# Optimization experiments

Hardware: AMD Instinct MI355X
Metric: run time of the kernel (lower is better)

The kernel has to match this reference:

```python
import jax, jax.numpy as jnp
import numpy as np

NUM_HEADS = 64          # also the positional-embedding size (quirk of the module)
DIM_IN, DIM_K, DIM_V = 512, 512, 64
BATCH, SEQ = 4, 1024


def setup_inputs() -> dict:
    key = jax.random.key(0)
    ks = jax.random.split(key, 7)
    s = 0.05  # weight init scale
    return {
        "x":  jax.random.normal(ks[0], (BATCH, SEQ, DIM_IN), jnp.float32),
        "Wq": jax.random.normal(ks[1], (DIM_IN, DIM_K), jnp.float32) * s,
        "bq": jax.random.normal(ks[2], (DIM_K,), jnp.float32) * s,
        "Wk": jax.random.normal(ks[3], (DIM_IN, DIM_K), jnp.float32) * s,
        "bk": jax.random.normal(ks[4], (DIM_K,), jnp.float32) * s,
        "Wv": jax.random.normal(ks[5], (DIM_IN, DIM_V), jnp.float32) * s,
        "bv": jax.random.normal(ks[6], (DIM_V,), jnp.float32) * s,
    }


def _position_embedding(n, position_size):
    # matches Position_Enbedding: cos block then sin block along feature dim
    half = position_size // 2
    pos_j = 1.0 / jnp.power(10000.0, 2.0 * jnp.arange(half, dtype=jnp.float32) / position_size)
    pos_ij = jnp.arange(n, dtype=jnp.float32)[:, None] * pos_j[None, :]   # [n, half]
    return jnp.concatenate([jnp.cos(pos_ij), jnp.sin(pos_ij)], axis=1)    # [n, position_size]


def reference(x, Wq, bq, Wk, bk, Wv, bv):
    B, n, _ = x.shape
    nh = NUM_HEADS
    dk = DIM_K // nh   # 8
    dv = DIM_V // nh   # 1
    # fused linear + ReLU, then split heads: [B, nh, n, d]
    q = jax.nn.relu(x @ Wq + bq).reshape(B, n, nh, dk).transpose(0, 2, 1, 3)
    k = jax.nn.relu(x @ Wk + bk).reshape(B, n, nh, dk).transpose(0, 2, 1, 3)
    v = jax.nn.relu(x @ Wv + bv).reshape(B, n, nh, dv).transpose(0, 2, 1, 3)
    scale = 1.0 / np.sqrt(dk).astype(np.float32)
    dist = jax.nn.softmax(jnp.einsum('bhqd,bhkd->bhqk', q, k) * scale, axis=-1)
    att = jnp.einsum('bhqk,bhkd->bhqd', dist, v)            # [B, nh, n, dv]
    att = att.transpose(0, 2, 1, 3).reshape(B, n, DIM_V)    # [B, n, dim_v]
    pe = _position_embedding(n, nh)                          # [n, nh] == [n, dim_v]
    return att + pe[None, :, :]
```

## Files before the change

kernel.cpp:

```cpp
#include <hip/hip_runtime.h>
#include <math.h>

#define BATCH 4
#define SEQ   1024
#define DIN   512
#define DKQ   512
#define DV    64
#define NH    64

typedef __attribute__((ext_vector_type(8))) short short8v;
typedef __attribute__((ext_vector_type(4))) float float4v;
typedef __attribute__((ext_vector_type(4))) unsigned int uint4v;

__device__ __forceinline__ void split_bf16(float f, unsigned short& hi, unsigned short& lo) {
    unsigned int u = __float_as_uint(f);
    hi = (unsigned short)(u >> 16);
    float l = f - __uint_as_float(u & 0xFFFF0000u);
    lo = (unsigned short)(__float_as_uint(l) >> 16);
}
__device__ __forceinline__ unsigned short f32_to_bf16_rne(float f) {
    unsigned int u = __float_as_uint(f);
    u += 0x7FFFu + ((u >> 16) & 1u);
    return (unsigned short)(u >> 16);
}
__device__ __forceinline__ float bf16_bits_to_f32(unsigned short s) {
    return __uint_as_float((unsigned int)s << 16);
}

__device__ __forceinline__ int ldsoff(int r, int sl) {
    return r * 64 + ((sl ^ (r & 7)) << 3);
}

__global__ __launch_bounds__(256)
void pack_x(const float* __restrict__ x,
            unsigned short* __restrict__ Xhi, unsigned short* __restrict__ Xlo)
{
    const int i = (blockIdx.x * 256 + threadIdx.x) * 8;
    float4 a0 = *(const float4*)&x[i];
    float4 a1 = *(const float4*)&x[i + 4];
    float av[8] = {a0.x, a0.y, a0.z, a0.w, a1.x, a1.y, a1.z, a1.w};
    short8v h, l;
    #pragma unroll
    for (int j = 0; j < 8; ++j) {
        unsigned short hh, ll; split_bf16(av[j], hh, ll);
        h[j] = (short)hh; l[j] = (short)ll;
    }
    *(short8v*)&Xhi[i] = h;
    *(short8v*)&Xlo[i] = l;
}

__global__ __launch_bounds__(256)
void transpose_w(const float* __restrict__ Wq, const float* __restrict__ Wk,
                 const float* __restrict__ Wv,
                 unsigned short* __restrict__ WhiQ, unsigned short* __restrict__ WloQ,
                 unsigned short* __restrict__ WhiK, unsigned short* __restrict__ WloK,
                 unsigned short* __restrict__ WhiV, unsigned short* __restrict__ WloV)
{
    const int z = blockIdx.z;
    const int N = (z == 2) ? DV : DKQ;
    if (z == 2 && blockIdx.x >= 2) return;
    const float* __restrict__ W = (z == 0) ? Wq : (z == 1) ? Wk : Wv;
    unsigned short* __restrict__ Whi = (z == 0) ? WhiQ : (z == 1) ? WhiK : WhiV;
    unsigned short* __restrict__ Wlo = (z == 0) ? WloQ : (z == 1) ? WloK : WloV;

    __shared__ float tile[32][33];
    const int n0 = blockIdx.x * 32, k0 = blockIdx.y * 32;
    const int tx = threadIdx.x, ty = threadIdx.y;
    #pragma unroll
    for (int i = 0; i < 32; i += 8)
        tile[ty + i][tx] = W[(size_t)(k0 + ty + i) * N + n0 + tx];
    __syncthreads();
    #pragma unroll
    for (int i = 0; i < 32; i += 8) {
        unsigned short h, l; split_bf16(tile[tx][ty + i], h, l);
        Whi[(size_t)(n0 + ty + i) * DIN + k0 + tx] = h;
        Wlo[(size_t)(n0 + ty + i) * DIN + k0 + tx] = l;
    }
}

__global__ __launch_bounds__(512)
void proj_kernel(const unsigned short* __restrict__ Xhi,
                 const unsigned short* __restrict__ Xlo,
                 const unsigned short* __restrict__ WhiQ, const unsigned short* __restrict__ WloQ,
                 const float* __restrict__ bq,
                 const unsigned short* __restrict__ WhiK, const unsigned short* __restrict__ WloK,
                 const float* __restrict__ bk,
                 const unsigned short* __restrict__ WhiV, const unsigned short* __restrict__ WloV,
                 const float* __restrict__ bv,
                 unsigned short* __restrict__ Qpk, unsigned short* __restrict__ Kpk,
                 unsigned int* __restrict__ Vhi, unsigned int* __restrict__ Vlo)
{
    const int z = blockIdx.z;
    if (z == 2 && blockIdx.x != 0) return;
    const unsigned short* __restrict__ Whi = (z == 0) ? WhiQ : (z == 1) ? WhiK : WhiV;
    const unsigned short* __restrict__ Wlo = (z == 0) ? WloQ : (z == 1) ? WloK : WloV;
    const float* __restrict__ bias = (z == 0) ? bq : (z == 1) ? bk : bv;

    __shared__ unsigned short As[128 * 64];
    __shared__ unsigned short Bs[128 * 64];

    const int t  = threadIdx.x;
    const int bm = blockIdx.y * 128;
    const int bn = blockIdx.x * 128;

    const int srow = t >> 2;
    const int sg   = t & 3;
    const bool bok = (z != 2) || (srow < 64);

    const int lane = t & 63, wave = t >> 6;
    const int wr = wave >> 2, wc = wave & 3;
    const int cl = lane & 15, g2 = lane >> 4;
    const int NF = (z == 2) ? 1 : 2;

    float4v acc[4][2];
    #pragma unroll
    for (int i = 0; i < 4; ++i)
        #pragma unroll
        for (int j = 0; j < 2; ++j)
            acc[i][j] = (float4v){0.f, 0.f, 0.f, 0.f};

    for (int ks = 0; ks < 16; ++ks) {
        const int k0 = ks * 32;
        const size_t ao = (size_t)(bm + srow) * DIN + k0 + sg * 8;
        short8v ahi = *(const short8v*)(Xhi + ao);
        short8v alo = *(const short8v*)(Xlo + ao);
        short8v bhi, blo;
        if (bok) {
            const size_t bo = (size_t)(bn + srow) * DIN + k0 + sg * 8;
            bhi = *(const short8v*)(Whi + bo);
            blo = *(const short8v*)(Wlo + bo);
        }
        __syncthreads();
        *(short8v*)&As[ldsoff(srow, sg * 2)]     = ahi;
        *(short8v*)&As[ldsoff(srow, sg * 2 + 1)] = alo;
        if (bok) {
            *(short8v*)&Bs[ldsoff(srow, sg * 2)]     = bhi;
            *(short8v*)&Bs[ldsoff(srow, sg * 2 + 1)] = blo;
        }
        __syncthreads();

        short8v af_h[4], af_l[4], bf_h[2], bf_l[2];
        #pragma unroll
        for (int mt = 0; mt < 4; ++mt) {
            const int r = wr * 64 + mt * 16 + cl;
            af_h[mt] = *(const short8v*)&As[ldsoff(r, g2 * 2)];
            af_l[mt] = *(const short8v*)&As[ldsoff(r, g2 * 2 + 1)];
        }
        #pragma unroll
        for (int nf = 0; nf < 2; ++nf) {
            if (nf < NF) {
                const int n = wc * (NF * 16) + nf * 16 + cl;
                bf_h[nf] = *(const short8v*)&Bs[ldsoff(n, g2 * 2)];
                bf_l[nf] = *(const short8v*)&Bs[ldsoff(n, g2 * 2 + 1)];
            }
        }
        #pragma unroll
        for (int mt = 0; mt < 4; ++mt)
            #pragma unroll
            for (int nf = 0; nf < 2; ++nf) {
                if (nf >= NF) continue;
                acc[mt][nf] = __builtin_amdgcn_mfma_f32_16x16x32_bf16(af_h[mt], bf_h[nf], acc[mt][nf], 0, 0, 0);
                acc[mt][nf] = __builtin_amdgcn_mfma_f32_16x16x32_bf16(af_l[mt], bf_h[nf], acc[mt][nf], 0, 0, 0);
                acc[mt][nf] = __builtin_amdgcn_mfma_f32_16x16x32_bf16(af_h[mt], bf_l[nf], acc[mt][nf], 0, 0, 0);
            }
    }

    const float cc = 0.35355339059327373f * 1.4426950408889634f;
    if (z == 2) {
        const int n = wc * 16 + cl;
        #pragma unroll
        for (int mt = 0; mt < 4; ++mt) {
            float vv[4]; unsigned short hh[4], ll[4];
            #pragma unroll
            for (int r = 0; r < 4; ++r) {
                vv[r] = fmaxf(acc[mt][0][r] + bias[n], 0.0f);
                hh[r] = f32_to_bf16_rne(vv[r]);
                ll[r] = f32_to_bf16_rne(vv[r] - bf16_bits_to_f32(hh[r]));
            }
            const int row0 = bm + wr * 64 + mt * 16 + g2 * 4;
            const int bb = row0 >> 10, s0 = row0 & 1023;
            size_t base = (size_t)((bb << 6) + n) * (SEQ / 2) + (s0 >> 1);
            Vhi[base]     = (unsigned int)hh[0] | ((unsigned int)hh[1] << 16);
            Vhi[base + 1] = (unsigned int)hh[2] | ((unsigned int)hh[3] << 16);
            Vlo[base]     = (unsigned int)ll[0] | ((unsigned int)ll[1] << 16);
            Vlo[base + 1] = (unsigned int)ll[2] | ((unsigned int)ll[3] << 16);
        }
    } else {
        #pragma unroll
        for (int mt = 0; mt < 4; ++mt) {
            #pragma unroll
            for (int nf = 0; nf < 2; ++nf) {
                #pragma unroll
                for (int r = 0; r < 4; ++r) {
                    const int row = bm + wr * 64 + mt * 16 + g2 * 4 + r;
                    const int bb = row >> 10, s = row & 1023;
                    const int n = bn + wc * 32 + nf * 16 + cl;
                    float val = fmaxf(acc[mt][nf][r] + bias[n], 0.0f);
                    if (z == 0) val *= cc;
                    const int hh2 = n >> 3, d = n & 7;
                    unsigned short* dst = (z == 0) ? Qpk : Kpk;
                    size_t base = ((size_t)((bb << 6) + hh2) * SEQ + s) * 16 + d;
                    unsigned short hi = f32_to_bf16_rne(val);
                    dst[base]     = hi;
                    dst[base + 8] = f32_to_bf16_rne(val - bf16_bits_to_f32(hi));
                }
            }
        }
    }
}

__global__ __launch_bounds__(256, 6)
void attn_kernel(const unsigned short* __restrict__ Qpk,
                 const unsigned short* __restrict__ Kpk,
                 const unsigned int* __restrict__ Vhi,
                 const unsigned int* __restrict__ Vlo,
                 float2* __restrict__ part)
{
    const int bh = blockIdx.x;
    const int yb = blockIdx.y;
    const int qchunk = yb >> 2;
    const int kq = yb & 3;
    const int t = threadIdx.x;
    const int wave = t >> 6, lane = t & 63;
    const int g = lane >> 4, cl = lane & 15;

    const unsigned short* __restrict__ qb = Qpk + (size_t)bh * SEQ * 16;
    const unsigned short* __restrict__ kb = Kpk + (size_t)bh * SEQ * 16;
    const unsigned int* __restrict__ vhb = Vhi + (size_t)bh * (SEQ / 2);
    const unsigned int* __restrict__ vlb = Vlo + (size_t)bh * (SEQ / 2);

    const int q0 = qchunk * 256 + wave * 64;

    short8v bq[4];
    #pragma unroll
    for (int qt = 0; qt < 4; ++qt) {
        if (g == 3) { short8v zz = {0,0,0,0,0,0,0,0}; bq[qt] = zz; }
        else bq[qt] = *(const short8v*)(qb + (size_t)(q0 + qt * 16 + cl) * 16 + ((g == 1) ? 8 : 0));
    }

    const int koff = (g >> 1) * 8;
    const unsigned int ONES = 0x3F803F80u;
    const float4v c0 = {0.f, 0.f, 0.f, 0.f};

    float4v acc[4];
    #pragma unroll
    for (int qt = 0; qt < 4; ++qt) acc[qt] = c0;

    const int nt0 = kq * 16;
    short8v kf = *(const short8v*)(kb + (size_t)(nt0 * 16 + cl) * 16 + koff);
    unsigned int vh0 = vhb[nt0 * 8 + g * 2], vh1 = vhb[nt0 * 8 + g * 2 + 1];
    unsigned int vl0 = vlb[nt0 * 8 + g * 2], vl1 = vlb[nt0 * 8 + g * 2 + 1];

    for (int nt = nt0; nt < nt0 + 16; ++nt) {
        const short8v kfc = kf;
        const unsigned int ch0 = vh0, ch1 = vh1, cll0 = vl0, cll1 = vl1;
        if (nt < nt0 + 15) {
            kf = *(const short8v*)(kb + (size_t)((nt + 1) * 16 + cl) * 16 + koff);
            vh0 = vhb[(nt + 1) * 8 + g * 2]; vh1 = vhb[(nt + 1) * 8 + g * 2 + 1];
            vl0 = vlb[(nt + 1) * 8 + g * 2]; vl1 = vlb[(nt + 1) * 8 + g * 2 + 1];
        }
        const unsigned int a0 = (cl == 0) ? ch0 : (cl == 1) ? ONES : (cl == 2) ? cll0 : 0u;
        const unsigned int a1 = (cl == 0) ? ch1 : (cl == 1) ? ONES : (cl == 2) ? cll1 : 0u;
        uint4v au = {a0, a1, 0u, 0u};
        const short8v af = __builtin_bit_cast(short8v, au);

        #pragma unroll
        for (int qt = 0; qt < 4; ++qt) {
            float4v st = __builtin_amdgcn_mfma_f32_16x16x32_bf16(kfc, bq[qt], c0, 0, 0, 0);
            float p0 = __builtin_amdgcn_exp2f(st[0]);
            float p1 = __builtin_amdgcn_exp2f(st[1]);
            float p2 = __builtin_amdgcn_exp2f(st[2]);
            float p3 = __builtin_amdgcn_exp2f(st[3]);
            unsigned int pk0 = __builtin_amdgcn_perm(__float_as_uint(p1), __float_as_uint(p0), 0x07060302u);
            unsigned int pk1 = __builtin_amdgcn_perm(__float_as_uint(p3), __float_as_uint(p2), 0x07060302u);
            uint4v pu = {pk0, pk1, 0u, 0u};
            acc[qt] = __builtin_amdgcn_mfma_f32_16x16x32_bf16(af, __builtin_bit_cast(short8v, pu), acc[qt], 0, 0, 0);
        }
    }

    if (g == 0) {
        #pragma unroll
        for (int qt = 0; qt < 4; ++qt) {
            const int row = q0 + qt * 16 + cl;
            float2 pr;
            pr.x = acc[qt][0] + acc[qt][2];
            pr.y = acc[qt][1];
            part[(size_t)(kq * 256 + bh) * SEQ + row] = pr;
        }
    }
}

__global__ __launch_bounds__(256)
void merge_kernel(const float2* __restrict__ part, float* __restrict__ out)
{
    const int tid = blockIdx.x * 256 + threadIdx.x;
    const int h = tid & 63;
    const int q = (tid >> 6) & 1023;
    const int b = tid >> 16;
    const int bh = (b << 6) + h;
    float num = 0.f, den = 0.f;
    #pragma unroll
    for (int kq = 0; kq < 4; ++kq) {
        float2 p = part[(size_t)(kq * 256 + bh) * SEQ + q];
        num += p.x; den += p.y;
    }
    const float fr = __builtin_amdgcn_exp2f((float)(h & 31) * -0.4152410118609203f);
    const float pe = (h < 32) ? cosf((float)q * fr) : sinf((float)q * fr);
    out[tid] = num / den + pe;
}

extern "C" void kernel_launch(void* const* d_in, const int* in_sizes, int n_in,
                              void* d_out, int out_size, void* d_ws, size_t ws_size,
                              hipStream_t stream)
{
    const float* x  = (const float*)d_in[0];
    const float* Wq = (const float*)d_in[1];
    const float* bq = (const float*)d_in[2];
    const float* Wk = (const float*)d_in[3];
    const float* bk = (const float*)d_in[4];
    const float* Wv = (const float*)d_in[5];
    const float* bv = (const float*)d_in[6];
    float* out = (float*)d_out;

    unsigned short* Qpk = (unsigned short*)d_ws;
    unsigned short* Kpk = Qpk + (size_t)BATCH * NH * SEQ * 16;
    unsigned int* Vhi = (unsigned int*)(Kpk + (size_t)BATCH * NH * SEQ * 16);
    unsigned int* Vlo = Vhi + (size_t)BATCH * NH * (SEQ / 2);
    unsigned short* Xhi = (unsigned short*)(Vlo + (size_t)BATCH * NH * (SEQ / 2));
    unsigned short* Xlo = Xhi + (size_t)BATCH * SEQ * DIN;
    float2* part = (float2*)Xhi;
    unsigned short* WhiQ = Xlo + (size_t)BATCH * SEQ * DIN;
    unsigned short* WloQ = WhiQ + (size_t)DIN * DKQ;
    unsigned short* WhiK = WloQ + (size_t)DIN * DKQ;
    unsigned short* WloK = WhiK + (size_t)DIN * DKQ;
    unsigned short* WhiV = WloK + (size_t)DIN * DKQ;
    unsigned short* WloV = WhiV + (size_t)DIN * DV;

    pack_x<<<dim3((BATCH * SEQ * DIN) / (8 * 256)), 256, 0, stream>>>(x, Xhi, Xlo);
    transpose_w<<<dim3(16, 16, 3), dim3(32, 8), 0, stream>>>(
        Wq, Wk, Wv, WhiQ, WloQ, WhiK, WloK, WhiV, WloV);
    proj_kernel<<<dim3(4, 32, 3), 512, 0, stream>>>(
        Xhi, Xlo, WhiQ, WloQ, bq, WhiK, WloK, bk, WhiV, WloV, bv, Qpk, Kpk, Vhi, Vlo);
    attn_kernel<<<dim3(256, 16), 256, 0, stream>>>(Qpk, Kpk, Vhi, Vlo, part);
    merge_kernel<<<dim3((BATCH * SEQ * DV) / 256), 256, 0, stream>>>(part, out);
}
```

Before: 86.18 us.

## Drop LDS staging in projection GEMM and process two key tiles per attention step

After: 115.8 us. 34.4% more time.

```diff
diff --git a/kernel.cpp b/kernel.cpp
--- a/kernel.cpp
+++ b/kernel.cpp
@@ -27,14 +27,13 @@
     return __uint_as_float((unsigned int)s << 16);
 }
 
-__device__ __forceinline__ int ldsoff(int r, int sl) {
-    return r * 64 + ((sl ^ (r & 7)) << 3);
-}
-
 __global__ __launch_bounds__(256)
 void pack_x(const float* __restrict__ x,
-            unsigned short* __restrict__ Xhi, unsigned short* __restrict__ Xlo)
-{
+            unsigned short* __restrict__ Xhi, unsigned short* __restrict__ Xlo,
+            unsigned int* __restrict__ obuf)
+{
+    if (blockIdx.x == 0 && threadIdx.x < 8)
+        obuf[threadIdx.x] = (threadIdx.x < 4) ? 0x3F803F80u : 0u;
     const int i = (blockIdx.x * 256 + threadIdx.x) * 8;
     float4 a0 = *(const float4*)&x[i];
     float4 a1 = *(const float4*)&x[i + 4];
@@ -78,7 +77,7 @@
     }
 }
 
-__global__ __launch_bounds__(512)
+__global__ __launch_bounds__(256)
 void proj_kernel(const unsigned short* __restrict__ Xhi,
                  const unsigned short* __restrict__ Xlo,
                  const unsigned short* __restrict__ WhiQ, const unsigned short* __restrict__ WloQ,
@@ -88,118 +87,125 @@
                  const unsigned short* __restrict__ WhiV, const unsigned short* __restrict__ WloV,
                  const float* __restrict__ bv,
                  unsigned short* __restrict__ Qpk, unsigned short* __restrict__ Kpk,
-                 unsigned int* __restrict__ Vhi, unsigned int* __restrict__ Vlo)
+                 unsigned int* __restrict__ Vsh, unsigned int* __restrict__ Vsl)
 {
     const int z = blockIdx.z;
-    if (z == 2 && blockIdx.x != 0) return;
+    const int t = threadIdx.x;
+    const int wave = t >> 6, lane = t & 63;
+    const int cl = lane & 15, g2 = lane >> 4;
+
+    int bm, cb;
+    if (z == 2) {
+        if (blockIdx.x != 0 || blockIdx.y >= 16) return;
+        bm = blockIdx.y * 256 + wave * 64;
+        cb = 0;
+    } else {
+        bm = blockIdx.y * 64;
+        cb = blockIdx.x * 256 + wave * 64;
+    }
     const unsigned short* __restrict__ Whi = (z == 0) ? WhiQ : (z == 1) ? WhiK : WhiV;
     const unsigned short* __restrict__ Wlo = (z == 0) ? WloQ : (z == 1) ? WloK : WloV;
     const float* __restrict__ bias = (z == 0) ? bq : (z == 1) ? bk : bv;
 
-    __shared__ unsigned short As[128 * 64];
-    __shared__ unsigned short Bs[128 * 64];
-
-    const int t  = threadIdx.x;
-    const int bm = blockIdx.y * 128;
-    const int bn = blockIdx.x * 128;
-
-    const int srow = t >> 2;
-    const int sg   = t & 3;
-    const bool bok = (z != 2) || (srow < 64);
-
-    const int lane = t & 63, wave = t >> 6;
-    const int wr = wave >> 2, wc = wave & 3;
-    const int cl = lane & 15, g2 = lane >> 4;
-    const int NF = (z == 2) ? 1 : 2;
-
-    float4v acc[4][2];
+    unsigned int aoff[4], boff[4];
+    #pragma unroll
+    for (int mt = 0; mt < 4; ++mt) aoff[mt] = (unsigned)(bm + mt * 16 + cl) * DIN + g2 * 8;
+    #pragma unroll
+    for (int nf = 0; nf < 4; ++nf) boff[nf] = (unsigned)(cb + nf * 16 + cl) * DIN + g2 * 8;
+
+    float4v acc[4][4];
     #pragma unroll
     for (int i = 0; i < 4; ++i)
         #pragma unroll
-        for (int j = 0; j < 2; ++j)
+        for (int j = 0; j < 4; ++j)
             acc[i][j] = (float4v){0.f, 0.f, 0.f, 0.f};
 
+    short8v Ah[2][4], Al[2][4], Bh[2][4], Bl[4];
+    #pragma unroll
+    for (int mt = 0; mt < 4; ++mt) {
+        Ah[0][mt] = *(const short8v*)(Xhi + aoff[mt]);
+        Al[0][mt] = *(const short8v*)(Xlo + aoff[mt]);
+    }
+    #pragma unroll
+    for (int nf = 0; nf < 4; ++nf)
+        Bh[0][nf] = *(const short8v*)(Whi + boff[nf]);
+
+    #pragma unroll
     for (int ks = 0; ks < 16; ++ks) {
-        const int k0 = ks * 32;
-        const size_t ao = (size_t)(bm + srow) * DIN + k0 + sg * 8;
-        short8v ahi = *(const short8v*)(Xhi + ao);
-        short8v alo = *(const short8v*)(Xlo + ao);
-        short8v bhi, blo;
-        if (bok) {
-            const size_t bo = (size_t)(bn + srow) * DIN + k0 + sg * 8;
-            bhi = *(const short8v*)(Whi + bo);
-            blo = *(const short8v*)(Wlo + bo);
-        }
-        __syncthreads();
-        *(short8v*)&As[ldsoff(srow, sg * 2)]     = ahi;
-        *(short8v*)&As[ldsoff(srow, sg * 2 + 1)] = alo;
-        if (bok) {
-            *(short8v*)&Bs[ldsoff(srow, sg * 2)]     = bhi;
-            *(short8v*)&Bs[ldsoff(srow, sg * 2 + 1)] = blo;
-        }
-        __syncthreads();
-
-        short8v af_h[4], af_l[4], bf_h[2], bf_l[2];
-        #pragma unroll
-        for (int mt = 0; mt < 4; ++mt) {
-            const int r = wr * 64 + mt * 16 + cl;
-            af_h[mt] = *(const short8v*)&As[ldsoff(r, g2 * 2)];
-            af_l[mt] = *(const short8v*)&As[ldsoff(r, g2 * 2 + 1)];
-        }
-        #pragma unroll
-        for (int nf = 0; nf < 2; ++nf) {
-            if (nf < NF) {
-                const int n = wc * (NF * 16) + nf * 16 + cl;
-                bf_h[nf] = *(const short8v*)&Bs[ldsoff(n, g2 * 2)];
-                bf_l[nf] = *(const short8v*)&Bs[ldsoff(n, g2 * 2 + 1)];
+        const int cur = ks & 1, nxt = cur ^ 1;
+        const int ko = ks * 32;
+        #pragma unroll
+        for (int nf = 0; nf < 4; ++nf)
+            Bl[nf] = *(const short8v*)(Wlo + boff[nf] + ko);
+        if (ks < 15) {
+            const int kn = ko + 32;
+            #pragma unroll
+            for (int mt = 0; mt < 4; ++mt) {
+                Ah[nxt][mt] = *(const short8v*)(Xhi + aoff[mt] + kn);
+                Al[nxt][mt] = *(const short8v*)(Xlo + aoff[mt] + kn);
             }
+            #pragma unroll
+            for (int nf = 0; nf < 4; ++nf)
+                Bh[nxt][nf] = *(const short8v*)(Whi + boff[nf] + kn);
         }
         #pragma unroll
         for (int mt = 0; mt < 4; ++mt)
             #pragma unroll
-            for (int nf = 0; nf < 2; ++nf) {
-                if (nf >= NF) continue;
-                acc[mt][nf] = __builtin_amdgcn_mfma_f32_16x16x32_bf16(af_h[mt], bf_h[nf], acc[mt][nf], 0, 0, 0);
-                acc[mt][nf] = __builtin_amdgcn_mfma_f32_16x16x32_bf16(af_l[mt], bf_h[nf], acc[mt][nf], 0, 0, 0);
-                acc[mt][nf] = __builtin_amdgcn_mfma_f32_16x16x32_bf16(af_h[mt], bf_l[nf], acc[mt][nf], 0, 0, 0);
-            }
+            for (int nf = 0; nf < 4; ++nf)
+                acc[mt][nf] = __builtin_amdgcn_mfma_f32_16x16x32_bf16(Ah[cur][mt], Bh[cur][nf], acc[mt][nf], 0, 0, 0);
+        #pragma unroll
+        for (int mt = 0; mt < 4; ++mt)
+            #pragma unroll
+            for (int nf = 0; nf < 4; ++nf)
+                acc[mt][nf] = __builtin_amdgcn_mfma_f32_16x16x32_bf16(Al[cur][mt], Bh[cur][nf], acc[mt][nf], 0, 0, 0);
+        #pragma unroll
+        for (int mt = 0; mt < 4; ++mt)
+            #pragma unroll
+            for (int nf = 0; nf < 4; ++nf)
+                acc[mt][nf] = __builtin_amdgcn_mfma_f32_16x16x32_bf16(Ah[cur][mt], Bl[nf], acc[mt][nf], 0, 0, 0);
     }
 
     const float cc = 0.35355339059327373f * 1.4426950408889634f;
     if (z == 2) {
-        const int n = wc * 16 + cl;
         #pragma unroll
         for (int mt = 0; mt < 4; ++mt) {
-            float vv[4]; unsigned short hh[4], ll[4];
-            #pragma unroll
-            for (int r = 0; r < 4; ++r) {
-                vv[r] = fmaxf(acc[mt][0][r] + bias[n], 0.0f);
-                hh[r] = f32_to_bf16_rne(vv[r]);
-                ll[r] = f32_to_bf16_rne(vv[r] - bf16_bits_to_f32(hh[r]));
-            }
-            const int row0 = bm + wr * 64 + mt * 16 + g2 * 4;
+            const int row0 = bm + mt * 16 + g2 * 4;
             const int bb = row0 >> 10, s0 = row0 & 1023;
-            size_t base = (size_t)((bb << 6) + n) * (SEQ / 2) + (s0 >> 1);
-            Vhi[base]     = (unsigned int)hh[0] | ((unsigned int)hh[1] << 16);
-            Vhi[base + 1] = (unsigned int)hh[2] | ((unsigned int)hh[3] << 16);
-            Vlo[base]     = (unsigned int)ll[0] | ((unsigned int)ll[1] << 16);
-            Vlo[base + 1] = (unsigned int)ll[2] | ((unsigned int)ll[3] << 16);
-        }
-    } else {
-        #pragma unroll
-        for (int mt = 0; mt < 4; ++mt) {
-            #pragma unroll
-            for (int nf = 0; nf < 2; ++nf) {
+            const int idx0 = (s0 >> 5) * 16 + ((s0 >> 2) & 3) * 4 + ((s0 >> 4) & 1) * 2;
+            #pragma unroll
+            for (int nf = 0; nf < 4; ++nf) {
+                const int n = nf * 16 + cl;
+                const float bn = bias[n];
+                float vv[4]; unsigned short hh[4], ll[4];
                 #pragma unroll
                 for (int r = 0; r < 4; ++r) {
-                    const int row = bm + wr * 64 + mt * 16 + g2 * 4 + r;
+                    vv[r] = fmaxf(acc[mt][nf][r] + bn, 0.0f);
+                    hh[r] = f32_to_bf16_rne(vv[r]);
+                    ll[r] = f32_to_bf16_rne(vv[r] - bf16_bits_to_f32(hh[r]));
+                }
+                const size_t base = (size_t)((bb << 6) + n) * 512 + idx0;
+                Vsh[base]     = (unsigned int)hh[0] | ((unsigned int)hh[1] << 16);
+                Vsh[base + 1] = (unsigned int)hh[2] | ((unsigned int)hh[3] << 16);
+                Vsl[base]     = (unsigned int)ll[0] | ((unsigned int)ll[1] << 16);
+                Vsl[base + 1] = (unsigned int)ll[2] | ((unsigned int)ll[3] << 16);
+            }
+        }
+    } else {
+        unsigned short* __restrict__ dst = (z == 0) ? Qpk : Kpk;
+        #pragma unroll
+        for (int nf = 0; nf < 4; ++nf) {
+            const int n = cb + nf * 16 + cl;
+            const float bn = bias[n];
+            const int h = n >> 3, d = n & 7;
+            #pragma unroll
+            for (int mt = 0; mt < 4; ++mt) {
+                #pragma unroll
+                for (int r = 0; r < 4; ++r) {
+                    const int row = bm + mt * 16 + g2 * 4 + r;
                     const int bb = row >> 10, s = row & 1023;
-                    const int n = bn + wc * 32 + nf * 16 + cl;
-                    float val = fmaxf(acc[mt][nf][r] + bias[n], 0.0f);
+                    float val = fmaxf(acc[mt][nf][r] + bn, 0.0f);
                     if (z == 0) val *= cc;
-                    const int hh2 = n >> 3, d = n & 7;
-                    unsigned short* dst = (z == 0) ? Qpk : Kpk;
-                    size_t base = ((size_t)((bb << 6) + hh2) * SEQ + s) * 16 + d;
+                    const size_t base = ((size_t)((bb << 6) + h) * SEQ + s) * 16 + d;
                     unsigned short hi = f32_to_bf16_rne(val);
                     dst[base]     = hi;
                     dst[base + 8] = f32_to_bf16_rne(val - bf16_bits_to_f32(hi));
@@ -209,11 +215,12 @@
     }
 }
 
-__global__ __launch_bounds__(256, 6)
+__global__ __launch_bounds__(256, 4)
 void attn_kernel(const unsigned short* __restrict__ Qpk,
                  const unsigned short* __restrict__ Kpk,
-                 const unsigned int* __restrict__ Vhi,
-                 const unsigned int* __restrict__ Vlo,
+                 const unsigned int* __restrict__ Vsh,
+                 const unsigned int* __restrict__ Vsl,
+                 const unsigned int* __restrict__ obuf,
                  float2* __restrict__ part)
 {
     const int bh = blockIdx.x;
@@ -226,8 +233,6 @@
 
     const unsigned short* __restrict__ qb = Qpk + (size_t)bh * SEQ * 16;
     const unsigned short* __restrict__ kb = Kpk + (size_t)bh * SEQ * 16;
-    const unsigned int* __restrict__ vhb = Vhi + (size_t)bh * (SEQ / 2);
-    const unsigned int* __restrict__ vlb = Vlo + (size_t)bh * (SEQ / 2);
 
     const int q0 = qchunk * 256 + wave * 64;
 
@@ -239,43 +244,57 @@
     }
 
     const int koff = (g >> 1) * 8;
-    const unsigned int ONES = 0x3F803F80u;
+    const unsigned short* kp = kb + kq * 4096 + cl * 16 + koff;
+
+    const unsigned int* ap;
+    int astr;
+    {
+        const size_t vb = (size_t)bh * 512 + kq * 128 + g * 4;
+        if (cl == 0)      { ap = Vsh + vb; astr = 16; }
+        else if (cl == 2) { ap = Vsl + vb; astr = 16; }
+        else if (cl == 1) { ap = obuf;     astr = 0;  }
+        else              { ap = obuf + 4; astr = 0;  }
+    }
+
     const float4v c0 = {0.f, 0.f, 0.f, 0.f};
-
     float4v acc[4];
     #pragma unroll
     for (int qt = 0; qt < 4; ++qt) acc[qt] = c0;
 
-    const int nt0 = kq * 16;
-    short8v kf = *(const short8v*)(kb + (size_t)(nt0 * 16 + cl) * 16 + koff);
-    unsigned int vh0 = vhb[nt0 * 8 + g * 2], vh1 = vhb[nt0 * 8 + g * 2 + 1];
-    unsigned int vl0 = vlb[nt0 * 8 + g * 2], vl1 = vlb[nt0 * 8 + g * 2 + 1];
-
-    for (int nt = nt0; nt < nt0 + 16; ++nt) {
-        const short8v kfc = kf;
-        const unsigned int ch0 = vh0, ch1 = vh1, cll0 = vl0, cll1 = vl1;
-        if (nt < nt0 + 15) {
-            kf = *(const short8v*)(kb + (size_t)((nt + 1) * 16 + cl) * 16 + koff);
-            vh0 = vhb[(nt + 1) * 8 + g * 2]; vh1 = vhb[(nt + 1) * 8 + g * 2 + 1];
-            vl0 = vlb[(nt + 1) * 8 + g * 2]; vl1 = vlb[(nt + 1) * 8 + g * 2 + 1];
-        }
-        const unsigned int a0 = (cl == 0) ? ch0 : (cl == 1) ? ONES : (cl == 2) ? cll0 : 0u;
-        const unsigned int a1 = (cl == 0) ? ch1 : (cl == 1) ? ONES : (cl == 2) ? cll1 : 0u;
-        uint4v au = {a0, a1, 0u, 0u};
-        const short8v af = __builtin_bit_cast(short8v, au);
-
+    short8v k0c = *(const short8v*)kp;
+    short8v k1c = *(const short8v*)(kp + 256);
+    uint4v  auc = *(const uint4v*)ap;
+
+    #pragma unroll
+    for (int ss = 0; ss < 8; ++ss) {
+        short8v k0n, k1n; uint4v aun;
+        if (ss < 7) {
+            k0n = *(const short8v*)(kp + 512);
+            k1n = *(const short8v*)(kp + 768);
+            aun = *(const uint4v*)(ap + astr);
+        }
+        kp += 512; ap += astr;
+        const short8v af = __builtin_bit_cast(short8v, auc);
         #pragma unroll
         for (int qt = 0; qt < 4; ++qt) {
-            float4v st = __builtin_amdgcn_mfma_f32_16x16x32_bf16(kfc, bq[qt], c0, 0, 0, 0);
-            float p0 = __builtin_amdgcn_exp2f(st[0]);
-            float p1 = __builtin_amdgcn_exp2f(st[1]);
-            float p2 = __builtin_amdgcn_exp2f(st[2]);
-            float p3 = __builtin_amdgcn_exp2f(st[3]);
-            unsigned int pk0 = __builtin_amdgcn_perm(__float_as_uint(p1), __float_as_uint(p0), 0x07060302u);
-            unsigned int pk1 = __builtin_amdgcn_perm(__float_as_uint(p3), __float_as_uint(p2), 0x07060302u);
-            uint4v pu = {pk0, pk1, 0u, 0u};
+            float4v s0 = __builtin_amdgcn_mfma_f32_16x16x32_bf16(k0c, bq[qt], c0, 0, 0, 0);
+            float4v s1 = __builtin_amdgcn_mfma_f32_16x16x32_bf16(k1c, bq[qt], c0, 0, 0, 0);
+            float p00 = __builtin_amdgcn_exp2f(s0[0]);
+            float p01 = __builtin_amdgcn_exp2f(s0[1]);
+            float p02 = __builtin_amdgcn_exp2f(s0[2]);
+            float p03 = __builtin_amdgcn_exp2f(s0[3]);
+            float p10 = __builtin_amdgcn_exp2f(s1[0]);
+            float p11 = __builtin_amdgcn_exp2f(s1[1]);
+            float p12 = __builtin_amdgcn_exp2f(s1[2]);
+            float p13 = __builtin_amdgcn_exp2f(s1[3]);
+            unsigned int pk0 = __builtin_amdgcn_perm(__float_as_uint(p01), __float_as_uint(p00), 0x07060302u);
+            unsigned int pk1 = __builtin_amdgcn_perm(__float_as_uint(p03), __float_as_uint(p02), 0x07060302u);
+            unsigned int pk2 = __builtin_amdgcn_perm(__float_as_uint(p11), __float_as_uint(p10), 0x07060302u);
+            unsigned int pk3 = __builtin_amdgcn_perm(__float_as_uint(p13), __float_as_uint(p12), 0x07060302u);
+            uint4v pu = {pk0, pk1, pk2, pk3};
             acc[qt] = __builtin_amdgcn_mfma_f32_16x16x32_bf16(af, __builtin_bit_cast(short8v, pu), acc[qt], 0, 0, 0);
         }
+        if (ss < 7) { k0c = k0n; k1c = k1n; auc = aun; }
     }
 
     if (g == 0) {
@@ -324,9 +343,10 @@
 
     unsigned short* Qpk = (unsigned short*)d_ws;
     unsigned short* Kpk = Qpk + (size_t)BATCH * NH * SEQ * 16;
-    unsigned int* Vhi = (unsigned int*)(Kpk + (size_t)BATCH * NH * SEQ * 16);
-    unsigned int* Vlo = Vhi + (size_t)BATCH * NH * (SEQ / 2);
-    unsigned short* Xhi = (unsigned short*)(Vlo + (size_t)BATCH * NH * (SEQ / 2));
+    unsigned int* Vsh = (unsigned int*)(Kpk + (size_t)BATCH * NH * SEQ * 16);
+    unsigned int* Vsl = Vsh + (size_t)BATCH * NH * (SEQ / 2);
+    unsigned int* obuf = Vsl + (size_t)BATCH * NH * (SEQ / 2);
+    unsigned short* Xhi = (unsigned short*)(obuf + 64);
     unsigned short* Xlo = Xhi + (size_t)BATCH * SEQ * DIN;
     float2* part = (float2*)Xhi;
     unsigned short* WhiQ = Xlo + (size_t)BATCH * SEQ * DIN;
@@ -336,11 +356,11 @@
     unsigned short* WhiV = WloK + (size_t)DIN * DKQ;
     unsigned short* WloV = WhiV + (size_t)DIN * DV;
 
-    pack_x<<<dim3((BATCH * SEQ * DIN) / (8 * 256)), 256, 0, stream>>>(x, Xhi, Xlo);
+    pack_x<<<dim3((BATCH * SEQ * DIN) / (8 * 256)), 256, 0, stream>>>(x, Xhi, Xlo, obuf);
     transpose_w<<<dim3(16, 16, 3), dim3(32, 8), 0, stream>>>(
         Wq, Wk, Wv, WhiQ, WloQ, WhiK, WloK, WhiV, WloV);
-    proj_kernel<<<dim3(4, 32, 3), 512, 0, stream>>>(
-        Xhi, Xlo, WhiQ, WloQ, bq, WhiK, WloK, bk, WhiV, WloV, bv, Qpk, Kpk, Vhi, Vlo);
-    attn_kernel<<<dim3(256, 16), 256, 0, stream>>>(Qpk, Kpk, Vhi, Vlo, part);
+    proj_kernel<<<dim3(2, 64, 3), 256, 0, stream>>>(
+        Xhi, Xlo, WhiQ, WloQ, bq, WhiK, WloK, bk, WhiV, WloV, bv, Qpk, Kpk, Vsh, Vsl);
+    attn_kernel<<<dim3(256, 16), 256, 0, stream>>>(Qpk, Kpk, Vsh, Vsl, obuf, part);
     merge_kernel<<<dim3((BATCH * SEQ * DV) / 256), 256, 0, stream>>>(part, out);
 }
```
